# Kernel tuning notes

Hardware: AMD Instinct MI355X
Metric: run time of the kernel (lower is better)

## Reference

```python
import jax, jax.numpy as jnp
import numpy as np

N, E = 100000, 600000
IN_DIM, HID, OUT_DIM = 128, 128, 1
BN_EPS = 1e-5
L2_EPS = 1e-12


def setup_inputs() -> dict:
    key = jax.random.key(0)
    ks = jax.random.split(key, 12)

    def xavier(k, shape):
        fan_in, fan_out = shape[0], shape[1]
        lim = float(np.sqrt(6.0 / (fan_in + fan_out)))
        return jax.random.uniform(k, shape, jnp.float32, -lim, lim)

    return {
        'x': jax.random.normal(ks[0], (N, IN_DIM), jnp.float32),
        'edge_index': jax.random.randint(ks[1], (2, E), 0, N, jnp.int32),
        # SAGEConv layer 1: lin_l (neighbor, with bias), lin_r (root, no bias)
        'W1_l': xavier(ks[2], (IN_DIM, HID)),
        'b1_l': jnp.zeros((HID,), jnp.float32),
        'W1_r': xavier(ks[3], (IN_DIM, HID)),
        # BatchNorm1d(hidden)
        'bn_gamma': jnp.ones((HID,), jnp.float32),
        'bn_beta': jnp.zeros((HID,), jnp.float32),
        # SAGEConv layer 2
        'W2_l': xavier(ks[4], (HID, HID)),
        'b2_l': jnp.zeros((HID,), jnp.float32),
        'W2_r': xavier(ks[5], (HID, HID)),
        # fc on causal half of embedding
        'fc_W': xavier(ks[6], (HID // 2, OUT_DIM)),
        'fc_b': jnp.zeros((OUT_DIM,), jnp.float32),
    }


def _sage_conv(x, src, dst, W_l, b_l, W_r, n_nodes):
    # mean-aggregate neighbor features: messages x[src] scattered to dst
    msg = x[src]  # [E, d] gather
    agg = jax.ops.segment_sum(msg, dst, num_segments=n_nodes)  # [N, d]
    cnt = jax.ops.segment_sum(jnp.ones((src.shape[0],), x.dtype), dst,
                              num_segments=n_nodes)  # [N]
    mean = agg / jnp.maximum(cnt, 1.0)[:, None]
    out = mean @ W_l + b_l + x @ W_r  # lin_l(agg) + lin_r(x)
    # normalize=True -> row-wise L2 normalize (F.normalize, eps=1e-12)
    nrm = jnp.linalg.norm(out, axis=-1, keepdims=True)
    return out / jnp.maximum(nrm, L2_EPS)


def reference(x, edge_index, W1_l, b1_l, W1_r, bn_gamma, bn_beta,
              W2_l, b2_l, W2_r, fc_W, fc_b):
    src, dst = edge_index[0], edge_index[1]
    n_nodes = x.shape[0]

    h = _sage_conv(x, src, dst, W1_l, b1_l, W1_r, n_nodes)

    # transition: ReLU -> BatchNorm1d (batch stats) -> Dropout (eval: identity)
    h = jax.nn.relu(h)
    mu = jnp.mean(h, axis=0)
    var = jnp.var(h, axis=0)
    h = (h - mu) * jax.lax.rsqrt(var + BN_EPS) * bn_gamma + bn_beta

    embed = _sage_conv(h, src, dst, W2_l, b2_l, W2_r, n_nodes)

    half = embed.shape[1] // 2
    preds = (embed[:, :half] @ fc_W + fc_b).squeeze()  # [N]
    return preds, embed
```

## Files before the change

kernel.cpp:

```cpp
#include <hip/hip_runtime.h>
#include <hip/hip_bf16.h>
#include <stdint.h>

typedef __attribute__((ext_vector_type(8))) __bf16 bf16x8;
typedef __attribute__((ext_vector_type(4))) float  f32x4;

__device__ __forceinline__ float bflo(uint32_t p){ return __uint_as_float(p << 16); }
__device__ __forceinline__ float bfhi(uint32_t p){ return __uint_as_float(p & 0xffff0000u); }
__device__ __forceinline__ uint16_t f2bf(float f){
    uint32_t u = __float_as_uint(f);
    uint32_t r = (u + 0x7fffu + ((u >> 16) & 1u)) >> 16;
    return (uint16_t)r;
}
__device__ __forceinline__ uint32_t packbf(float a, float b){
    return (uint32_t)f2bf(a) | ((uint32_t)f2bf(b) << 16);
}
__device__ __forceinline__ f32x4 MFMA(bf16x8 a, bf16x8 b, f32x4 c){
    return __builtin_amdgcn_mfma_f32_16x16x32_bf16(a, b, c, 0, 0, 0);
}

#define MB_IDX(row, lane) ((size_t)(row) * 128 + 64 + (lane))

__global__ void k_deg(const int* __restrict__ dst, int* __restrict__ counts, int E){
    int e = blockIdx.x * 256 + threadIdx.x;
    if (e < E) atomicAdd(&counts[dst[e]], 1);
}

__global__ void k_scan1(const int* __restrict__ counts, int* __restrict__ bsums, int N){
    __shared__ int lds[256];
    int t = threadIdx.x;
    int base = blockIdx.x * 2048 + t * 8;
    int s = 0;
    #pragma unroll
    for (int i = 0; i < 8; ++i){ int idx = base + i; s += (idx < N) ? counts[idx] : 0; }
    lds[t] = s; __syncthreads();
    for (int off = 128; off > 0; off >>= 1){
        if (t < off) lds[t] += lds[t + off];
        __syncthreads();
    }
    if (t == 0) bsums[blockIdx.x] = lds[0];
}

__global__ void k_scan2(int* bsums, int NB){
    int run = 0;
    for (int i = 0; i < NB; ++i){ int v = bsums[i]; bsums[i] = run; run += v; }
}

__global__ void k_scan3(const int* __restrict__ counts, const int* __restrict__ bsums,
                        int* __restrict__ offs, int N){
    __shared__ int lds[256];
    int t = threadIdx.x;
    int base = blockIdx.x * 2048 + t * 8;
    int local[8];
    int s = 0;
    #pragma unroll
    for (int i = 0; i < 8; ++i){
        int idx = base + i;
        int v = (idx < N) ? counts[idx] : 0;
        local[i] = v; s += v;
    }
    lds[t] = s; __syncthreads();
    for (int off = 1; off < 256; off <<= 1){
        int v = (t >= off) ? lds[t - off] : 0;
        __syncthreads();
        lds[t] += v;
        __syncthreads();
    }
    int run = bsums[blockIdx.x] + (lds[t] - s);
    #pragma unroll
    for (int i = 0; i < 8; ++i){
        int idx = base + i;
        if (idx < N){ offs[idx] = run; run += local[i]; }
    }
}

__global__ void k_fill(const int* __restrict__ src, const int* __restrict__ dst,
                       const int* __restrict__ offs, int* __restrict__ cursor,
                       int* __restrict__ ssrc, int E){
    int e = blockIdx.x * 256 + threadIdx.x;
    if (e < E){
        int d = dst[e];
        int p = atomicAdd(&cursor[d], 1);
        ssrc[offs[d] + p] = src[e];
    }
}

__global__ __launch_bounds__(256) void k_x2bf(const float* __restrict__ X,
        uint32_t* __restrict__ XbfE, uint32_t* __restrict__ Xlo, int N){
    int i = blockIdx.x * 256 + threadIdx.x;
    if (i >= N * 64) return;
    int row = i >> 6, lane = i & 63;
    float2 v = *(const float2*)(X + (size_t)i * 2);
    uint16_t h0 = f2bf(v.x), h1 = f2bf(v.y);
    float r0 = v.x - __uint_as_float((uint32_t)h0 << 16);
    float r1 = v.y - __uint_as_float((uint32_t)h1 << 16);
    XbfE[(size_t)row * 128 + lane] = (uint32_t)h0 | ((uint32_t)h1 << 16);
    Xlo[(size_t)i] = packbf(r0, r1);
}

__global__ void k_wprep(const float* __restrict__ Wl, const float* __restrict__ Wr,
                        const float* __restrict__ scale,
                        uint16_t* __restrict__ Wpk){
    int idx = blockIdx.x * 256 + threadIdx.x;
    int c = idx >> 8, k = idx & 255;
    float v;
    if (k < 128){
        v = Wl[k * 128 + c];
    } else {
        v = Wr[(k - 128) * 128 + c];
        if (scale) v *= scale[k - 128];
    }
    uint16_t h = f2bf(v);
    float r = v - __uint_as_float((uint32_t)h << 16);
    int kt = k >> 5, kk = k & 31;
    int g = kk >> 3, e = kk & 7;
    int slot = (c << 2) | (g ^ ((c >> 1) & 3));
    size_t base = (size_t)kt * 8192 + (size_t)slot * 8 + e;
    Wpk[base]        = h;
    Wpk[base + 4096] = f2bf(r);
}

template<int MODE>
__global__ __launch_bounds__(256) void k_agg(
        const uint32_t* __restrict__ Src, int sstr,
        const int* __restrict__ offs, const int* __restrict__ counts,
        const int* __restrict__ ssrc,
        const float* __restrict__ bnscale, const float* __restrict__ bnshift,
        uint32_t* __restrict__ MbBase, int N){
    int lane = threadIdx.x & 63;
    int node = blockIdx.x * 4 + (threadIdx.x >> 6);
    if (node >= N) return;
    int cnt = counts[node];
    if (cnt < 0) cnt = 0;
    int off = offs[node];
    float a0 = 0.f, a1 = 0.f;
    int j = 0;
    for (; j + 4 <= cnt; j += 4){
        int s0 = ssrc[off + j];
        int s1 = ssrc[off + j + 1];
        int s2 = ssrc[off + j + 2];
        int s3 = ssrc[off + j + 3];
        s0 = (s0 < 0) ? 0 : ((s0 >= N) ? (N - 1) : s0);
        s1 = (s1 < 0) ? 0 : ((s1 >= N) ? (N - 1) : s1);
        s2 = (s2 < 0) ? 0 : ((s2 >= N) ? (N - 1) : s2);
        s3 = (s3 < 0) ? 0 : ((s3 >= N) ? (N - 1) : s3);
        uint32_t p0 = Src[(size_t)s0 * sstr + lane];
        uint32_t p1 = Src[(size_t)s1 * sstr + lane];
        uint32_t p2 = Src[(size_t)s2 * sstr + lane];
        uint32_t p3 = Src[(size_t)s3 * sstr + lane];
        a0 += bflo(p0) + bflo(p1) + bflo(p2) + bflo(p3);
        a1 += bfhi(p0) + bfhi(p1) + bfhi(p2) + bfhi(p3);
    }
    for (; j < cnt; ++j){
        int s = ssrc[off + j];
        s = (s < 0) ? 0 : ((s >= N) ? (N - 1) : s);
        uint32_t p = Src[(size_t)s * sstr + lane];
        a0 += bflo(p); a1 += bfhi(p);
    }
    float inv = 1.0f / fmaxf((float)cnt, 1.0f);
    a0 *= inv; a1 *= inv;
    if (MODE == 1){
        int c0 = lane * 2;
        float sh0 = (cnt > 0) ? bnshift[c0]     : 0.f;
        float sh1 = (cnt > 0) ? bnshift[c0 + 1] : 0.f;
        a0 = a0 * bnscale[c0]     + sh0;
        a1 = a1 * bnscale[c0 + 1] + sh1;
    }
    MbBase[MB_IDX(node, lane)] = packbf(a0, a1);
}

__device__ __forceinline__ void stage_sel(const uint32_t* Wpk, uint32_t (*sB)[2048],
                                          int wid, int lane, int sel){
    #pragma unroll
    for (int i = 0; i < 16; ++i){
        int ch = wid * 16 + i;
        int ktv = ch >> 3, part = ch & 7;
        __builtin_amdgcn_global_load_lds(
            Wpk + ktv * 4096 + sel * 2048 + part * 256 + lane * 4,
            &sB[ktv][part * 256], 16, 0, 0);
    }
}

template<int MODE>
__global__ __launch_bounds__(256, 2) void k_gemm(
        const uint32_t* Own,
        const uint32_t* OwnLo,
        const uint32_t* Mb,
        const uint32_t* __restrict__ Wpk,
        const float* __restrict__ bias,
        uint32_t* HbfOut,
        float* Emb,
        float* __restrict__ bnsum, float* __restrict__ bnsumsq,
        const float* __restrict__ fcW, const float* __restrict__ fcb,
        float* __restrict__ preds, int N){
    __shared__ uint32_t __align__(16) sB[8][2048];
    const int lane = threadIdx.x & 63;
    const int wid  = threadIdx.x >> 6;
    const int l15  = lane & 15;
    const int g    = lane >> 4;
    const int gx4  = (g ^ ((l15 >> 1) & 3)) * 4;
    const int ostr = (MODE == 0) ? 128 : 64;
    const int rowb = blockIdx.x * 128 + wid * 32;

    stage_sel(Wpk, sB, wid, lane, 0);

    int ar0 = rowb + l15;      if (ar0 >= N) ar0 = N - 1;
    int ar1 = rowb + 16 + l15; if (ar1 >= N) ar1 = N - 1;

    const uint32_t* mp0 = Mb  + (size_t)ar0 * 128 + 64 + g * 4;
    const uint32_t* mp1 = Mb  + (size_t)ar1 * 128 + 64 + g * 4;
    const uint32_t* op0 = Own + (size_t)ar0 * ostr + g * 4;
    const uint32_t* op1 = Own + (size_t)ar1 * ostr + g * 4;

    bf16x8 am0[4], am1[4], ao0[4], ao1[4];
    #pragma unroll
    for (int q = 0; q < 4; ++q){
        am0[q] = *(const bf16x8*)(mp0 + q * 16);
        am1[q] = *(const bf16x8*)(mp1 + q * 16);
        ao0[q] = *(const bf16x8*)(op0 + q * 16);
        ao1[q] = *(const bf16x8*)(op1 + q * 16);
    }
    bf16x8 xl0[4], xl1[4];
    if (MODE == 0){
        #pragma unroll
        for (int q = 0; q < 4; ++q){
            xl0[q] = *(const bf16x8*)(OwnLo + (size_t)ar0 * 64 + g * 4 + q * 16);
            xl1[q] = *(const bf16x8*)(OwnLo + (size_t)ar1 * 64 + g * 4 + q * 16);
        }
    }

    f32x4 acc0[8], acc1[8];
    const f32x4 zero = {0.f, 0.f, 0.f, 0.f};
    #pragma unroll
    for (int t = 0; t < 8; ++t){ acc0[t] = zero; acc1[t] = zero; }

    __syncthreads();

    #pragma unroll
    for (int kt = 0; kt < 8; ++kt){
        bf16x8 a0 = (kt < 4) ? am0[kt] : ao0[kt - 4];
        bf16x8 a1 = (kt < 4) ? am1[kt] : ao1[kt - 4];
        #pragma unroll
        for (int t = 0; t < 8; ++t){
            bf16x8 bh = *(const bf16x8*)(&sB[kt][(t * 16 + l15) * 16 + gx4]);
            acc0[t] = MFMA(a0, bh, acc0[t]);
            acc1[t] = MFMA(a1, bh, acc1[t]);
            if (MODE == 0 && kt >= 4){
                acc0[t] = MFMA(xl0[kt - 4], bh, acc0[t]);
                acc1[t] = MFMA(xl1[kt - 4], bh, acc1[t]);
            }
        }
    }

    __syncthreads();
    stage_sel(Wpk, sB, wid, lane, 1);
    __syncthreads();

    #pragma unroll
    for (int kt = 0; kt < 8; ++kt){
        bf16x8 a0 = (kt < 4) ? am0[kt] : ao0[kt - 4];
        bf16x8 a1 = (kt < 4) ? am1[kt] : ao1[kt - 4];
        #pragma unroll
        for (int t = 0; t < 8; ++t){
            bf16x8 bl = *(const bf16x8*)(&sB[kt][(t * 16 + l15) * 16 + gx4]);
            acc0[t] = MFMA(a0, bl, acc0[t]);
            acc1[t] = MFMA(a1, bl, acc1[t]);
        }
    }

    float bv[8];
    #pragma unroll
    for (int t = 0; t < 8; ++t) bv[t] = bias[t * 16 + l15];

    float fw[4]; float fb = 0.f;
    if (MODE == 1){
        #pragma unroll
        for (int t = 0; t < 4; ++t) fw[t] = fcW[t * 16 + l15];
        fb = fcb[0];
    }

    float pbs[8], pbq[8];
    #pragma unroll
    for (int t = 0; t < 8; ++t){ pbs[t] = 0.f; pbq[t] = 0.f; }

    #pragma unroll
    for (int m = 0; m < 2; ++m){
        #pragma unroll
        for (int j = 0; j < 4; ++j){
            int orow = rowb + m * 16 + 4 * g + j;
            bool valid = orow < N;
            float o[8]; float ss = 0.f;
            #pragma unroll
            for (int t = 0; t < 8; ++t){
                o[t] = (m == 0 ? acc0[t][j] : acc1[t][j]) + bv[t];
                ss += o[t] * o[t];
            }
            ss += __shfl_xor(ss, 1, 64);
            ss += __shfl_xor(ss, 2, 64);
            ss += __shfl_xor(ss, 4, 64);
            ss += __shfl_xor(ss, 8, 64);
            float inv = 1.0f / fmaxf(sqrtf(ss), 1e-12f);
            if (MODE == 0){
                #pragma unroll
                for (int t = 0; t < 8; ++t){
                    float v = fmaxf(o[t] * inv, 0.f);
                    float pv = __shfl_xor(v, 1, 64);
                    if (valid){
                        pbs[t] += v; pbq[t] += v * v;
                        if (!(lane & 1))
                            HbfOut[(size_t)orow * 64 + t * 8 + (l15 >> 1)] = packbf(v, pv);
                    }
                }
            } else {
                float p = 0.f;
                #pragma unroll
                for (int t = 0; t < 8; ++t){
                    float v = o[t] * inv;
                    if (valid) Emb[(size_t)orow * 128 + t * 16 + l15] = v;
                    if (t < 4) p += v * fw[t];
                }
                p += __shfl_xor(p, 1, 64);
                p += __shfl_xor(p, 2, 64);
                p += __shfl_xor(p, 4, 64);
                p += __shfl_xor(p, 8, 64);
                if (valid && l15 == 0) preds[orow] = p + fb;
            }
        }
    }

    if (MODE == 0){
        float* lsum = (float*)&sB[0][0];
        float* lsq  = lsum + 128;
        #pragma unroll
        for (int t = 0; t < 8; ++t){
            pbs[t] += __shfl_xor(pbs[t], 16, 64);
            pbs[t] += __shfl_xor(pbs[t], 32, 64);
            pbq[t] += __shfl_xor(pbq[t], 16, 64);
            pbq[t] += __shfl_xor(pbq[t], 32, 64);
        }
        __syncthreads();
        if (threadIdx.x < 128){ lsum[threadIdx.x] = 0.f; lsq[threadIdx.x] = 0.f; }
        __syncthreads();
        if (lane < 16){
            #pragma unroll
            for (int t = 0; t < 8; ++t){
                atomicAdd(&lsum[t * 16 + lane], pbs[t]);
                atomicAdd(&lsq [t * 16 + lane], pbq[t]);
            }
        }
        __syncthreads();
        if (threadIdx.x < 128){
            atomicAdd(&bnsum[threadIdx.x],   lsum[threadIdx.x]);
            atomicAdd(&bnsumsq[threadIdx.x], lsq[threadIdx.x]);
        }
    }
}

__global__ void k_bnfinal(const float* __restrict__ bnsum, const float* __restrict__ bnsumsq,
                          const float* __restrict__ gamma, const float* __restrict__ beta,
                          const float* __restrict__ W2r, const float* __restrict__ b2,
                          float* __restrict__ scale, float* __restrict__ shift,
                          float* __restrict__ bias2, int N){
    __shared__ float sh_l[128];
    int t = threadIdx.x;
    float invN = 1.0f / (float)N;
    float mu  = bnsum[t] * invN;
    float var = fmaxf(bnsumsq[t] * invN - mu * mu, 0.f);
    float istd = 1.0f / sqrtf(var + 1e-5f);
    float sc = gamma[t] * istd;
    float sf = beta[t] - mu * sc;
    scale[t] = sc; shift[t] = sf; sh_l[t] = sf;
    __syncthreads();
    float acc = b2[t];
    for (int k = 0; k < 128; ++k) acc += sh_l[k] * W2r[k * 128 + t];
    bias2[t] = acc;
}

__global__ void k_sent(float* __restrict__ preds, int N, float val){
    int i = blockIdx.x * 256 + threadIdx.x;
    if (i < N) preds[i] = val;
}

extern "C" void kernel_launch(void* const* d_in, const int* in_sizes, int n_in,
                              void* d_out, int out_size, void* d_ws, size_t ws_size,
                              hipStream_t stream){
    const int N = in_sizes[0] / 128;
    const int E = in_sizes[1] / 2;

    const float* x    = (const float*)d_in[0];
    const int*   ei   = (const int*)d_in[1];
    const int*   src  = ei;
    const int*   dst  = ei + E;
    const float* W1l  = (const float*)d_in[2];
    const float* b1   = (const float*)d_in[3];
    const float* W1r  = (const float*)d_in[4];
    const float* gam  = (const float*)d_in[5];
    const float* bet  = (const float*)d_in[6];
    const float* W2l  = (const float*)d_in[7];
    const float* b2   = (const float*)d_in[8];
    const float* W2r  = (const float*)d_in[9];
    const float* fcW  = (const float*)d_in[10];
    const float* fcb  = (const float*)d_in[11];

    float* preds = (float*)d_out;
    float* Emb   = preds + N;
    uint32_t* EmbU = (uint32_t*)Emb;

    char* w = (char*)d_ws;
    auto carve = [&](size_t bytes){ char* p = w; w += (bytes + 255) & ~(size_t)255; return p; };
    int*   counts  = (int*)  carve((size_t)N * 4);
    int*   offs    = (int*)  carve((size_t)N * 4);
    int*   cursor  = (int*)  carve((size_t)N * 4);
    int*   bsums   = (int*)  carve(256 * 4);
    float* bnsum   = (float*)carve(128 * 4);
    float* bnsumsq = (float*)carve(128 * 4);
    float* bnscale = (float*)carve(128 * 4);
    float* bnshift = (float*)carve(128 * 4);
    float* bias2   = (float*)carve(128 * 4);
    int*   ssrc    = (int*)  carve((size_t)E * 4);
    uint32_t* HbfXlo = (uint32_t*)carve((size_t)N * 256);
    uint16_t* Wpk1 = (uint16_t*)carve(131072);
    uint16_t* Wpk2 = (uint16_t*)carve(131072);
    size_t need = (size_t)(w - (char*)d_ws);
    if (ws_size < need){
        float val = 1024.f + 4.f * (float)((ws_size >> 20) > 255 ? 255 : (ws_size >> 20));
        k_sent<<<(N + 255) / 256, 256, 0, stream>>>(preds, N, val);
        return;
    }

    hipMemsetAsync(counts, 0, (size_t)N * 4, stream);
    hipMemsetAsync(cursor, 0, (size_t)N * 4, stream);
    hipMemsetAsync(bnsum,  0, 1024, stream);

    const int eb = (E + 255) / 256;
    const int NB = (N + 2047) / 2048;
    const int ab = (N + 3) / 4;
    const int gb = (N + 127) / 128;
    const int xb = (N * 64 + 255) / 256;

    k_deg  <<<eb, 256, 0, stream>>>(dst, counts, E);
    k_scan1<<<NB, 256, 0, stream>>>(counts, bsums, N);
    k_scan2<<<1,    1, 0, stream>>>(bsums, NB);
    k_scan3<<<NB, 256, 0, stream>>>(counts, bsums, offs, N);
    k_fill <<<eb, 256, 0, stream>>>(src, dst, offs, cursor, ssrc, E);

    k_x2bf <<<xb, 256, 0, stream>>>(x, EmbU, HbfXlo, N);
    k_wprep<<<128, 256, 0, stream>>>(W1l, W1r, nullptr, Wpk1);

    k_agg<0> <<<ab, 256, 0, stream>>>(EmbU, 128, offs, counts, ssrc,
                                      nullptr, nullptr, EmbU, N);
    k_gemm<0><<<gb, 256, 0, stream>>>(EmbU, HbfXlo, EmbU, (const uint32_t*)Wpk1, b1,
                                      HbfXlo, nullptr, bnsum, bnsumsq,
                                      nullptr, nullptr, nullptr, N);
    k_bnfinal<<<1, 128, 0, stream>>>(bnsum, bnsumsq, gam, bet, W2r, b2,
                                     bnscale, bnshift, bias2, N);
    k_wprep<<<128, 256, 0, stream>>>(W2l, W2r, bnscale, Wpk2);

    k_agg<1> <<<ab, 256, 0, stream>>>(HbfXlo, 64, offs, counts, ssrc,
                                      bnscale, bnshift, EmbU, N);
    k_gemm<1><<<gb, 256, 0, stream>>>(HbfXlo, nullptr, EmbU, (const uint32_t*)Wpk2, bias2,
                                      nullptr, Emb, nullptr, nullptr,
                                      fcW, fcb, preds, N);
}
```

Baseline: 376.5 us.

## Vectorize gather/convert kernels and halve GEMM LDS footprint for occupancy

The aggregation kernel now has each quarter-wave load a 16-byte chunk of a neighbor row, so four neighbors are gathered per wave instruction, then reduces across quarters with shuffles and writes one uint4 per node. The fp32-to-bf16 conversion uses float4 loads and uint2 stores. The GEMM stages weights in four 32KB chunks instead of two 64KB halves, which allows launch bounds of 4 blocks per CU at the cost of more barriers and restaging. The counts and cursor buffers are also merged so a single memset clears both.

```diff
diff --git a/kernel.cpp b/kernel.cpp
--- a/kernel.cpp
+++ b/kernel.cpp
@@ -88,14 +88,19 @@
 __global__ __launch_bounds__(256) void k_x2bf(const float* __restrict__ X,
         uint32_t* __restrict__ XbfE, uint32_t* __restrict__ Xlo, int N){
     int i = blockIdx.x * 256 + threadIdx.x;
-    if (i >= N * 64) return;
-    int row = i >> 6, lane = i & 63;
-    float2 v = *(const float2*)(X + (size_t)i * 2);
-    uint16_t h0 = f2bf(v.x), h1 = f2bf(v.y);
+    if (i >= N * 32) return;
+    int row = i >> 5, l = i & 31;
+    float4 v = *(const float4*)(X + (size_t)i * 4);
+    uint16_t h0 = f2bf(v.x), h1 = f2bf(v.y), h2 = f2bf(v.z), h3 = f2bf(v.w);
     float r0 = v.x - __uint_as_float((uint32_t)h0 << 16);
     float r1 = v.y - __uint_as_float((uint32_t)h1 << 16);
-    XbfE[(size_t)row * 128 + lane] = (uint32_t)h0 | ((uint32_t)h1 << 16);
-    Xlo[(size_t)i] = packbf(r0, r1);
+    float r2 = v.z - __uint_as_float((uint32_t)h2 << 16);
+    float r3 = v.w - __uint_as_float((uint32_t)h3 << 16);
+    uint2 hi; hi.x = (uint32_t)h0 | ((uint32_t)h1 << 16);
+    hi.y = (uint32_t)h2 | ((uint32_t)h3 << 16);
+    uint2 lo; lo.x = packbf(r0, r1); lo.y = packbf(r2, r3);
+    *(uint2*)(XbfE + (size_t)row * 128 + l * 2) = hi;
+    *(uint2*)(Xlo  + (size_t)row * 64  + l * 2) = lo;
 }
 
 __global__ void k_wprep(const float* __restrict__ Wl, const float* __restrict__ Wr,
@@ -127,62 +132,102 @@
         const int* __restrict__ ssrc,
         const float* __restrict__ bnscale, const float* __restrict__ bnshift,
         uint32_t* __restrict__ MbBase, int N){
-    int lane = threadIdx.x & 63;
+    const int lane = threadIdx.x & 63;
+    const int l15  = lane & 15;
+    const int q    = lane >> 4;
     int node = blockIdx.x * 4 + (threadIdx.x >> 6);
     if (node >= N) return;
     int cnt = counts[node];
     if (cnt < 0) cnt = 0;
     int off = offs[node];
-    float a0 = 0.f, a1 = 0.f;
+    const uint32_t* srcb = Src + l15 * 4;
+    float a[8];
+    #pragma unroll
+    for (int i = 0; i < 8; ++i) a[i] = 0.f;
+
     int j = 0;
-    for (; j + 4 <= cnt; j += 4){
-        int s0 = ssrc[off + j];
-        int s1 = ssrc[off + j + 1];
-        int s2 = ssrc[off + j + 2];
-        int s3 = ssrc[off + j + 3];
+    for (; j + 8 <= cnt; j += 8){
+        int s0 = ssrc[off + j + q];
+        int s1 = ssrc[off + j + 4 + q];
         s0 = (s0 < 0) ? 0 : ((s0 >= N) ? (N - 1) : s0);
         s1 = (s1 < 0) ? 0 : ((s1 >= N) ? (N - 1) : s1);
-        s2 = (s2 < 0) ? 0 : ((s2 >= N) ? (N - 1) : s2);
-        s3 = (s3 < 0) ? 0 : ((s3 >= N) ? (N - 1) : s3);
-        uint32_t p0 = Src[(size_t)s0 * sstr + lane];
-        uint32_t p1 = Src[(size_t)s1 * sstr + lane];
-        uint32_t p2 = Src[(size_t)s2 * sstr + lane];
-        uint32_t p3 = Src[(size_t)s3 * sstr + lane];
-        a0 += bflo(p0) + bflo(p1) + bflo(p2) + bflo(p3);
-        a1 += bfhi(p0) + bfhi(p1) + bfhi(p2) + bfhi(p3);
-    }
-    for (; j < cnt; ++j){
-        int s = ssrc[off + j];
-        s = (s < 0) ? 0 : ((s >= N) ? (N - 1) : s);
-        uint32_t p = Src[(size_t)s * sstr + lane];
-        a0 += bflo(p); a1 += bfhi(p);
+        uint4 v0 = *(const uint4*)(srcb + (size_t)s0 * sstr);
+        uint4 v1 = *(const uint4*)(srcb + (size_t)s1 * sstr);
+        a[0] += bflo(v0.x) + bflo(v1.x); a[1] += bfhi(v0.x) + bfhi(v1.x);
+        a[2] += bflo(v0.y) + bflo(v1.y); a[3] += bfhi(v0.y) + bfhi(v1.y);
+        a[4] += bflo(v0.z) + bflo(v1.z); a[5] += bfhi(v0.z) + bfhi(v1.z);
+        a[6] += bflo(v0.w) + bflo(v1.w); a[7] += bfhi(v0.w) + bfhi(v1.w);
+    }
+    int rem = cnt - j;
+    if (rem > 0){
+        if (q < rem){
+            int s0 = ssrc[off + j + q];
+            s0 = (s0 < 0) ? 0 : ((s0 >= N) ? (N - 1) : s0);
+            uint4 v0 = *(const uint4*)(srcb + (size_t)s0 * sstr);
+            a[0] += bflo(v0.x); a[1] += bfhi(v0.x);
+            a[2] += bflo(v0.y); a[3] += bfhi(v0.y);
+            a[4] += bflo(v0.z); a[5] += bfhi(v0.z);
+            a[6] += bflo(v0.w); a[7] += bfhi(v0.w);
+        }
+        if (rem > 4 && q < rem - 4){
+            int s1 = ssrc[off + j + 4 + q];
+            s1 = (s1 < 0) ? 0 : ((s1 >= N) ? (N - 1) : s1);
+            uint4 v1 = *(const uint4*)(srcb + (size_t)s1 * sstr);
+            a[0] += bflo(v1.x); a[1] += bfhi(v1.x);
+            a[2] += bflo(v1.y); a[3] += bfhi(v1.y);
+            a[4] += bflo(v1.z); a[5] += bfhi(v1.z);
+            a[6] += bflo(v1.w); a[7] += bfhi(v1.w);
+        }
+    }
+
+    #pragma unroll
+    for (int i = 0; i < 8; ++i){
+        a[i] += __shfl_xor(a[i], 16, 64);
+        a[i] += __shfl_xor(a[i], 32, 64);
     }
     float inv = 1.0f / fmaxf((float)cnt, 1.0f);
-    a0 *= inv; a1 *= inv;
+    #pragma unroll
+    for (int i = 0; i < 8; ++i) a[i] *= inv;
+
     if (MODE == 1){
-        int c0 = lane * 2;
-        float sh0 = (cnt > 0) ? bnshift[c0]     : 0.f;
-        float sh1 = (cnt > 0) ? bnshift[c0 + 1] : 0.f;
-        a0 = a0 * bnscale[c0]     + sh0;
-        a1 = a1 * bnscale[c0 + 1] + sh1;
-    }
-    MbBase[MB_IDX(node, lane)] = packbf(a0, a1);
-}
-
-__device__ __forceinline__ void stage_sel(const uint32_t* Wpk, uint32_t (*sB)[2048],
-                                          int wid, int lane, int sel){
-    #pragma unroll
-    for (int i = 0; i < 16; ++i){
-        int ch = wid * 16 + i;
+        if (cnt > 0){
+            int c0 = l15 * 8;
+            float4 sc0 = *(const float4*)(bnscale + c0);
+            float4 sc1 = *(const float4*)(bnscale + c0 + 4);
+            float4 sh0 = *(const float4*)(bnshift + c0);
+            float4 sh1 = *(const float4*)(bnshift + c0 + 4);
+            a[0] = a[0] * sc0.x + sh0.x; a[1] = a[1] * sc0.y + sh0.y;
+            a[2] = a[2] * sc0.z + sh0.z; a[3] = a[3] * sc0.w + sh0.w;
+            a[4] = a[4] * sc1.x + sh1.x; a[5] = a[5] * sc1.y + sh1.y;
+            a[6] = a[6] * sc1.z + sh1.z; a[7] = a[7] * sc1.w + sh1.w;
+        } else {
+            #pragma unroll
+            for (int i = 0; i < 8; ++i) a[i] = 0.f;
+        }
+    }
+
+    if (q == 0){
+        uint4 o;
+        o.x = packbf(a[0], a[1]); o.y = packbf(a[2], a[3]);
+        o.z = packbf(a[4], a[5]); o.w = packbf(a[6], a[7]);
+        *(uint4*)(MbBase + (size_t)node * 128 + 64 + l15 * 4) = o;
+    }
+}
+
+__device__ __forceinline__ void stage4(const uint32_t* Wpk, uint32_t (*sB)[2048],
+                                       int wid, int lane, int sel, int half){
+    #pragma unroll
+    for (int i = 0; i < 8; ++i){
+        int ch = wid * 8 + i;
         int ktv = ch >> 3, part = ch & 7;
         __builtin_amdgcn_global_load_lds(
-            Wpk + ktv * 4096 + sel * 2048 + part * 256 + lane * 4,
+            Wpk + (size_t)(half * 4 + ktv) * 4096 + sel * 2048 + part * 256 + lane * 4,
             &sB[ktv][part * 256], 16, 0, 0);
     }
 }
 
 template<int MODE>
-__global__ __launch_bounds__(256, 2) void k_gemm(
+__global__ __launch_bounds__(256, 4) void k_gemm(
         const uint32_t* Own,
         const uint32_t* OwnLo,
         const uint32_t* Mb,
@@ -193,7 +238,7 @@
         float* __restrict__ bnsum, float* __restrict__ bnsumsq,
         const float* __restrict__ fcW, const float* __restrict__ fcb,
         float* __restrict__ preds, int N){
-    __shared__ uint32_t __align__(16) sB[8][2048];
+    __shared__ uint32_t __align__(16) sB[4][2048];
     const int lane = threadIdx.x & 63;
     const int wid  = threadIdx.x >> 6;
     const int l15  = lane & 15;
@@ -202,7 +247,7 @@
     const int ostr = (MODE == 0) ? 128 : 64;
     const int rowb = blockIdx.x * 128 + wid * 32;
 
-    stage_sel(Wpk, sB, wid, lane, 0);
+    stage4(Wpk, sB, wid, lane, 0, 0);
 
     int ar0 = rowb + l15;      if (ar0 >= N) ar0 = N - 1;
     int ar1 = rowb + 16 + l15; if (ar1 >= N) ar1 = N - 1;
@@ -214,18 +259,18 @@
 
     bf16x8 am0[4], am1[4], ao0[4], ao1[4];
     #pragma unroll
-    for (int q = 0; q < 4; ++q){
-        am0[q] = *(const bf16x8*)(mp0 + q * 16);
-        am1[q] = *(const bf16x8*)(mp1 + q * 16);
-        ao0[q] = *(const bf16x8*)(op0 + q * 16);
-        ao1[q] = *(const bf16x8*)(op1 + q * 16);
+    for (int kq = 0; kq < 4; ++kq){
+        am0[kq] = *(const bf16x8*)(mp0 + kq * 16);
+        am1[kq] = *(const bf16x8*)(mp1 + kq * 16);
+        ao0[kq] = *(const bf16x8*)(op0 + kq * 16);
+        ao1[kq] = *(const bf16x8*)(op1 + kq * 16);
     }
     bf16x8 xl0[4], xl1[4];
     if (MODE == 0){
         #pragma unroll
-        for (int q = 0; q < 4; ++q){
-            xl0[q] = *(const bf16x8*)(OwnLo + (size_t)ar0 * 64 + g * 4 + q * 16);
-            xl1[q] = *(const bf16x8*)(OwnLo + (size_t)ar1 * 64 + g * 4 + q * 16);
+        for (int kq = 0; kq < 4; ++kq){
+            xl0[kq] = *(const bf16x8*)(OwnLo + (size_t)ar0 * 64 + g * 4 + kq * 16);
+            xl1[kq] = *(const bf16x8*)(OwnLo + (size_t)ar1 * 64 + g * 4 + kq * 16);
         }
     }
 
@@ -234,39 +279,36 @@
     #pragma unroll
     for (int t = 0; t < 8; ++t){ acc0[t] = zero; acc1[t] = zero; }
 
-    __syncthreads();
-
-    #pragma unroll
-    for (int kt = 0; kt < 8; ++kt){
-        bf16x8 a0 = (kt < 4) ? am0[kt] : ao0[kt - 4];
-        bf16x8 a1 = (kt < 4) ? am1[kt] : ao1[kt - 4];
-        #pragma unroll
-        for (int t = 0; t < 8; ++t){
-            bf16x8 bh = *(const bf16x8*)(&sB[kt][(t * 16 + l15) * 16 + gx4]);
-            acc0[t] = MFMA(a0, bh, acc0[t]);
-            acc1[t] = MFMA(a1, bh, acc1[t]);
-            if (MODE == 0 && kt >= 4){
-                acc0[t] = MFMA(xl0[kt - 4], bh, acc0[t]);
-                acc1[t] = MFMA(xl1[kt - 4], bh, acc1[t]);
-            }
-        }
-    }
-
-    __syncthreads();
-    stage_sel(Wpk, sB, wid, lane, 1);
-    __syncthreads();
-
-    #pragma unroll
-    for (int kt = 0; kt < 8; ++kt){
-        bf16x8 a0 = (kt < 4) ? am0[kt] : ao0[kt - 4];
-        bf16x8 a1 = (kt < 4) ? am1[kt] : ao1[kt - 4];
-        #pragma unroll
-        for (int t = 0; t < 8; ++t){
-            bf16x8 bl = *(const bf16x8*)(&sB[kt][(t * 16 + l15) * 16 + gx4]);
-            acc0[t] = MFMA(a0, bl, acc0[t]);
-            acc1[t] = MFMA(a1, bl, acc1[t]);
-        }
-    }
+#define COMPUTE4(AM0, AM1, ADD_XLO)                                           \
+    _Pragma("unroll")                                                         \
+    for (int kk = 0; kk < 4; ++kk){                                           \
+        _Pragma("unroll")                                                     \
+        for (int t = 0; t < 8; ++t){                                          \
+            bf16x8 bq = *(const bf16x8*)(&sB[kk][(t * 16 + l15) * 16 + gx4]); \
+            acc0[t] = MFMA(AM0[kk], bq, acc0[t]);                             \
+            acc1[t] = MFMA(AM1[kk], bq, acc1[t]);                             \
+            if (ADD_XLO){                                                     \
+                acc0[t] = MFMA(xl0[kk], bq, acc0[t]);                         \
+                acc1[t] = MFMA(xl1[kk], bq, acc1[t]);                         \
+            }                                                                 \
+        }                                                                     \
+    }
+
+    __syncthreads();
+    COMPUTE4(am0, am1, false);
+    __syncthreads();
+    stage4(Wpk, sB, wid, lane, 0, 1);
+    __syncthreads();
+    COMPUTE4(ao0, ao1, (MODE == 0));
+    __syncthreads();
+    stage4(Wpk, sB, wid, lane, 1, 0);
+    __syncthreads();
+    COMPUTE4(am0, am1, false);
+    __syncthreads();
+    stage4(Wpk, sB, wid, lane, 1, 1);
+    __syncthreads();
+    COMPUTE4(ao0, ao1, false);
+#undef COMPUTE4
 
     float bv[8];
     #pragma unroll
@@ -408,9 +450,9 @@
 
     char* w = (char*)d_ws;
     auto carve = [&](size_t bytes){ char* p = w; w += (bytes + 255) & ~(size_t)255; return p; };
-    int*   counts  = (int*)  carve((size_t)N * 4);
+    int*   counts  = (int*)  carve((size_t)N * 8);
+    int*   cursor  = counts + N;
     int*   offs    = (int*)  carve((size_t)N * 4);
-    int*   cursor  = (int*)  carve((size_t)N * 4);
     int*   bsums   = (int*)  carve(256 * 4);
     float* bnsum   = (float*)carve(128 * 4);
     float* bnsumsq = (float*)carve(128 * 4);
@@ -428,15 +470,14 @@
         return;
     }
 
-    hipMemsetAsync(counts, 0, (size_t)N * 4, stream);
-    hipMemsetAsync(cursor, 0, (size_t)N * 4, stream);
+    hipMemsetAsync(counts, 0, (size_t)N * 8, stream);
     hipMemsetAsync(bnsum,  0, 1024, stream);
 
     const int eb = (E + 255) / 256;
     const int NB = (N + 2047) / 2048;
     const int ab = (N + 3) / 4;
     const int gb = (N + 127) / 128;
-    const int xb = (N * 64 + 255) / 256;
+    const int xb = (N * 32 + 255) / 256;
 
     k_deg  <<<eb, 256, 0, stream>>>(dst, counts, E);
     k_scan1<<<NB, 256, 0, stream>>>(counts, bsums, N);
```

Result: slower. 386.4 us (+2.6%).
